# Optimization experiments

Hardware: AMD Instinct MI355X
Metric: run time of the kernel (lower is better)

## Reference

```python
import jax, jax.numpy as jnp
import numpy as np

N_TOKENS = 32768   # flattened batch*seq tokens
D = 1024           # expert_dim
E = 8              # num_experts
K = 2              # top_k


def setup_inputs() -> dict:
    key = jax.random.key(0)
    k0, k1, k2, k3, k4 = jax.random.split(key, 5)
    s = 1.0 / np.sqrt(D)  # torch Linear default init scale
    x = jax.random.normal(k0, (N_TOKENS, D), dtype=jnp.float32)
    gate_W = jax.random.normal(k1, (E, D), dtype=jnp.float32) * s
    gate_b = jax.random.uniform(k2, (E,), dtype=jnp.float32, minval=-s, maxval=s)
    expert_W = jax.random.normal(k3, (E, D, D), dtype=jnp.float32) * s
    expert_b = jax.random.uniform(k4, (E, D), dtype=jnp.float32, minval=-s, maxval=s)
    return {"x": x, "gate_W": gate_W, "gate_b": gate_b,
            "expert_W": expert_W, "expert_b": expert_b}


def reference(x, gate_W, gate_b, expert_W, expert_b):
    # Gating: logits [N, E] -> softmax -> top-k selection.
    logits = x @ gate_W.T + gate_b
    probs = jax.nn.softmax(logits, axis=-1)
    _, topk_idx = jax.lax.top_k(probs, K)                      # [N, K]
    # Combine weight = full softmax prob (NOT renormalized), zero if not in top-k.
    topk_mask = jax.nn.one_hot(topk_idx, E, dtype=probs.dtype).sum(axis=1)  # [N, E]
    w = probs * topk_mask                                       # [N, E]
    # Dense weighted dispatch/combine: mathematically identical to the
    # gather -> Linear -> scale -> scatter-add loop (w is 0 for unrouted experts).
    out = jnp.zeros_like(x)
    for e in range(E):  # fixed small structural loop over experts
        y_e = x @ expert_W[e].T + expert_b[e]                   # [N, D]
        out = out + w[:, e:e + 1] * y_e
    return out
```

## Files before the change

### kernel.cpp

```cpp
#include <hip/hip_runtime.h>
#include <hip/hip_bf16.h>
#include <cstdint>


#define N_TOK 32768
#define DIM   1024
#define NEXP  8
#define BM    128
#define BK    32
#define NTM   263

typedef __attribute__((ext_vector_type(8))) short short8;
typedef __attribute__((ext_vector_type(4))) float f32x4;
typedef unsigned short u16;

struct Ctrl {
  int counts[16];
  int cursors[16];
  int ntiles[2];
  int pad[30];
  int4 table[2 * NTM];
};

__device__ __forceinline__ void gload_lds16(void* lds, const void* g) {
  __builtin_amdgcn_global_load_lds(
      (const __attribute__((address_space(1))) void*)g,
      (__attribute__((address_space(3))) void*)lds, 16, 0, 0);
}

__device__ __forceinline__ void splitf(float f, u16& h, u16& l) {
  uint32_t u = __float_as_uint(f);
  h = (u16)(u >> 16);
  float r = f - __uint_as_float(u & 0xFFFF0000u);
  l = (u16)(__float_as_uint(r) >> 16);
}

extern "C" __global__ __launch_bounds__(256) void k_convert_w(
    const float4* __restrict__ W, ushort4* __restrict__ Wh, ushort4* __restrict__ Wl) {
  const int total = NEXP * DIM * DIM / 4;
  for (int i = blockIdx.x * 256 + threadIdx.x; i < total; i += gridDim.x * 256) {
    float4 v = W[i];
    u16 hx, lx, hy, ly, hz, lz, hw, lw;
    splitf(v.x, hx, lx); splitf(v.y, hy, ly);
    splitf(v.z, hz, lz); splitf(v.w, hw, lw);
    Wh[i] = make_ushort4(hx, hy, hz, hw);
    Wl[i] = make_ushort4(lx, ly, lz, lw);
  }
}

extern "C" __global__ __launch_bounds__(256) void k_gate(
    const float* __restrict__ x, const float* __restrict__ gW,
    const float* __restrict__ gb, u16* __restrict__ xh, u16* __restrict__ xl,
    float* __restrict__ wts, int* __restrict__ eids, int* __restrict__ counts) {
  __shared__ float4 gwl[NEXP * 256];
  __shared__ int cnt[16];
  int tid = threadIdx.x;
  for (int i = tid; i < NEXP * 256; i += 256) gwl[i] = ((const float4*)gW)[i];
  if (tid < 16) cnt[tid] = 0;
  __syncthreads();

  float gbr[NEXP];
#pragma unroll
  for (int e = 0; e < NEXP; ++e) gbr[e] = gb[e];

  int lane = tid & 63, wid = tid >> 6;
  int wave = blockIdx.x * 4 + wid;
  for (int t = wave; t < N_TOK; t += 2048) {
    const float4* xr = (const float4*)(x + (size_t)t * DIM);
    float acc[NEXP] = {0,0,0,0,0,0,0,0};
    float4 xv[4];
#pragma unroll
    for (int j = 0; j < 4; ++j) {
      float4 v = xr[j * 64 + lane];
      xv[j] = v;
#pragma unroll
      for (int e = 0; e < NEXP; ++e) {
        float4 g = gwl[e * 256 + j * 64 + lane];
        acc[e] += v.x * g.x + v.y * g.y + v.z * g.z + v.w * g.w;
      }
    }
#pragma unroll
    for (int off = 32; off > 0; off >>= 1)
#pragma unroll
      for (int e = 0; e < NEXP; ++e) acc[e] += __shfl_xor(acc[e], off, 64);

#pragma unroll
    for (int e = 0; e < NEXP; ++e) acc[e] += gbr[e];

    float m = acc[0];
#pragma unroll
    for (int e = 1; e < NEXP; ++e) m = fmaxf(m, acc[e]);
    float p[NEXP], s = 0.f;
#pragma unroll
    for (int e = 0; e < NEXP; ++e) { p[e] = expf(acc[e] - m); s += p[e]; }
    float inv = 1.f / s;

    int i0 = 0; float b0 = acc[0];
#pragma unroll
    for (int e = 1; e < NEXP; ++e) if (acc[e] > b0) { b0 = acc[e]; i0 = e; }
    int i1 = -1; float b1 = -3.4e38f;
#pragma unroll
    for (int e = 0; e < NEXP; ++e)
      if (e != i0 && acc[e] > b1) { b1 = acc[e]; i1 = e; }

    if (lane == 0) {
      wts[t * 2 + 0] = p[i0] * inv;
      wts[t * 2 + 1] = p[i1] * inv;
      eids[t * 2 + 0] = i0;
      eids[t * 2 + 1] = i1;
      atomicAdd(&cnt[i0], 1);
      atomicAdd(&cnt[8 + i1], 1);
    }
    ushort4* oh = (ushort4*)(xh + (size_t)t * DIM);
    ushort4* ol = (ushort4*)(xl + (size_t)t * DIM);
#pragma unroll
    for (int j = 0; j < 4; ++j) {
      u16 hx, lx, hy, ly, hz, lz, hw, lw;
      splitf(xv[j].x, hx, lx); splitf(xv[j].y, hy, ly);
      splitf(xv[j].z, hz, lz); splitf(xv[j].w, hw, lw);
      oh[j * 64 + lane] = make_ushort4(hx, hy, hz, hw);
      ol[j * 64 + lane] = make_ushort4(lx, ly, lz, lw);
    }
  }
  __syncthreads();
  if (tid < 16) atomicAdd(&counts[tid], cnt[tid]);
}

extern "C" __global__ void k_scan(Ctrl* ctrl) {
  if (threadIdx.x == 0) {
    for (int s = 0; s < 2; ++s) {
      int off = 0, nt = 0;
      for (int e = 0; e < NEXP; ++e) {
        int c = ctrl->counts[s * 8 + e];
        ctrl->cursors[s * 8 + e] = off;
        int tcnt = (c + BM - 1) >> 7;
        for (int i = 0; i < tcnt; ++i)
          ctrl->table[s * NTM + nt + i] =
              make_int4(e, off + i * BM, min(BM, c - i * BM), 0);
        nt += tcnt; off += c;
      }
      ctrl->ntiles[s] = nt;
    }
  }
}

extern "C" __global__ __launch_bounds__(256) void k_lists(
    const int* __restrict__ eids, int* __restrict__ cursors, int* __restrict__ lists) {
  int t = blockIdx.x * 256 + threadIdx.x;
  int lane = threadIdx.x & 63;
#pragma unroll
  for (int s = 0; s < 2; ++s) {
    int e = eids[t * 2 + s];
#pragma unroll
    for (int ex = 0; ex < NEXP; ++ex) {
      unsigned long long msk = __ballot(e == ex);
      if (msk) {
        int leader = __ffsll((unsigned long long)msk) - 1;
        int base = 0;
        if (lane == leader) base = atomicAdd(&cursors[s * 8 + ex], (int)__popcll(msk));
        base = __shfl(base, leader, 64);
        if (e == ex) {
          int pos = base + (int)__popcll(msk & ((1ull << lane) - 1ull));
          lists[s * N_TOK + pos] = t;
        }
      }
    }
  }
}

extern "C" __global__ __launch_bounds__(256) void k_gemm(
    int slot, const u16* __restrict__ xh, const u16* __restrict__ xl,
    const u16* __restrict__ Wh, const u16* __restrict__ Wl,
    const float* __restrict__ eb, const float* __restrict__ wts,
    const int* __restrict__ lists, const int* __restrict__ ntiles,
    const int4* __restrict__ table, float* __restrict__ out) {
  int tm = blockIdx.x >> 3, tn = blockIdx.x & 7;
  if (tm >= ntiles[slot]) return;
  int4 ent = table[slot * NTM + tm];
  int e = ent.x, start = ent.y, rows = ent.z;
  int n0 = tn * 128;

  __shared__ __align__(16) u16 Al[BM * BK];
  __shared__ __align__(16) u16 Bl[BM * BK];
  __shared__ int   tok[BM];
  __shared__ float wt[BM];

  int tid = threadIdx.x;
  if (tid < BM) {
    int t = 0; float w = 0.f;
    if (tid < rows) {
      t = lists[slot * N_TOK + start + tid];
      w = wts[t * 2 + slot];
    }
    tok[tid] = t; wt[tid] = w;
  }
  __syncthreads();

  int lane = tid & 63, wid = tid >> 6;
  int r0 = tid >> 2, seg = (tid & 3) * 8;
  int r1 = (tid + 256) >> 2;
  size_t aoff0 = (size_t)tok[r0] * DIM + seg;
  size_t aoff1 = (size_t)tok[r1] * DIM + seg;
  size_t boff0 = ((size_t)e * DIM + (n0 + r0)) * DIM + seg;
  size_t boff1 = ((size_t)e * DIM + (n0 + r1)) * DIM + seg;
  char* a_dst0 = (char*)Al + wid * 1024;
  char* a_dst1 = (char*)Al + 4096 + wid * 1024;
  char* b_dst0 = (char*)Bl + wid * 1024;
  char* b_dst1 = (char*)Bl + 4096 + wid * 1024;

  f32x4 acc[4][4] = {};
  int wm = wid >> 1, wn = wid & 1;
  int lrow = lane & 15, lk = (lane >> 4) * 8;

#pragma unroll 1
  for (int term = 0; term < 3; ++term) {
    const u16* asrc = (term == 2) ? xl : xh;
    const u16* bsrc = (term == 1) ? Wl : Wh;
    const u16* ap0 = asrc + aoff0;
    const u16* ap1 = asrc + aoff1;
    const u16* bp0 = bsrc + boff0;
    const u16* bp1 = bsrc + boff1;
#pragma unroll 1
    for (int col = 0; col < DIM; col += BK) {
      gload_lds16(a_dst0, ap0 + col);
      gload_lds16(a_dst1, ap1 + col);
      gload_lds16(b_dst0, bp0 + col);
      gload_lds16(b_dst1, bp1 + col);
      __syncthreads();

      short8 a[4], b[4];
#pragma unroll
      for (int mi = 0; mi < 4; ++mi)
        a[mi] = *(const short8*)&Al[(wm * 64 + mi * 16 + lrow) * BK + lk];
#pragma unroll
      for (int ni = 0; ni < 4; ++ni)
        b[ni] = *(const short8*)&Bl[(wn * 64 + ni * 16 + lrow) * BK + lk];
#pragma unroll
      for (int mi = 0; mi < 4; ++mi)
#pragma unroll
        for (int ni = 0; ni < 4; ++ni)
          acc[mi][ni] = __builtin_amdgcn_mfma_f32_16x16x32_bf16(
              a[mi], b[ni], acc[mi][ni], 0, 0, 0);
      __syncthreads();
    }
  }

#pragma unroll
  for (int mi = 0; mi < 4; ++mi) {
    int rbase = wm * 64 + mi * 16 + (lane >> 4) * 4;
#pragma unroll
    for (int ni = 0; ni < 4; ++ni) {
      int c = n0 + wn * 64 + ni * 16 + (lane & 15);
      float bv = eb[e * DIM + c];
#pragma unroll
      for (int j = 0; j < 4; ++j) {
        int r = rbase + j;
        if (r < rows) {
          float v = wt[r] * (acc[mi][ni][j] + bv);
          size_t oidx = (size_t)tok[r] * DIM + c;
          if (slot == 0) out[oidx] = v;
          else           out[oidx] += v;
        }
      }
    }
  }
}

extern "C" void kernel_launch(void* const* d_in, const int* in_sizes, int n_in,
                              void* d_out, int out_size, void* d_ws, size_t ws_size,
                              hipStream_t stream) {
  const float* x  = (const float*)d_in[0];
  const float* gW = (const float*)d_in[1];
  const float* gb = (const float*)d_in[2];
  const float* eW = (const float*)d_in[3];
  const float* eb = (const float*)d_in[4];
  float* out = (float*)d_out;

  char* ws = (char*)d_ws;
  size_t o = 0;
  u16* xh = (u16*)(ws + o); o += (size_t)N_TOK * DIM * 2;
  u16* xl = (u16*)(ws + o); o += (size_t)N_TOK * DIM * 2;
  u16* Wh = (u16*)(ws + o); o += (size_t)NEXP * DIM * DIM * 2;
  u16* Wl = (u16*)(ws + o); o += (size_t)NEXP * DIM * DIM * 2;
  float* wts = (float*)(ws + o); o += (size_t)N_TOK * 2 * 4;
  int* eids  = (int*)(ws + o);   o += (size_t)N_TOK * 2 * 4;
  int* lists = (int*)(ws + o);   o += (size_t)2 * N_TOK * 4;
  Ctrl* ctrl = (Ctrl*)(ws + o);  o += sizeof(Ctrl);

  hipMemsetAsync(ctrl->counts, 0, 16 * sizeof(int), stream);

  k_convert_w<<<2048, 256, 0, stream>>>((const float4*)eW, (ushort4*)Wh, (ushort4*)Wl);
  k_gate<<<512, 256, 0, stream>>>(x, gW, gb, xh, xl, wts, eids, ctrl->counts);
  k_scan<<<1, 64, 0, stream>>>(ctrl);
  k_lists<<<N_TOK / 256, 256, 0, stream>>>(eids, ctrl->cursors, lists);
  k_gemm<<<NTM * 8, 256, 0, stream>>>(0, xh, xl, Wh, Wl, eb, wts, lists,
                                      ctrl->ntiles, ctrl->table, out);
  k_gemm<<<NTM * 8, 256, 0, stream>>>(1, xh, xl, Wh, Wl, eb, wts, lists,
                                      ctrl->ntiles, ctrl->table, out);
}
```

Baseline: 1.102 ms.

## Rewrite grouped GEMM with 256x256 tiles, 4-stage LDS pipeline and swizzle

The grouped expert GEMM moves from 128x128 tiles with 256 threads and a synchronous single-buffer K loop to 256x256 tiles with 512 threads. It now runs a 4-deep global-to-LDS prefetch ring over a flattened 96-step K loop covering all three split-bf16 terms, uses an XOR swizzle on LDS offsets, and overlaps loads with MFMA half-steps using barriers, waitcnt and setprio. Blocks are remapped so neighbouring blocks share expert tiles, and the counts memset is folded into the weight-convert kernel. The aim is more data reuse per tile and hidden memory latency. The cost is 128KB of LDS per block, heavy register use, and more padding waste in expert tiles that are only partly filled.

```diff
diff --git a/kernel.cpp b/kernel.cpp
--- a/kernel.cpp
+++ b/kernel.cpp
@@ -6,9 +6,7 @@
 #define N_TOK 32768
 #define DIM   1024
 #define NEXP  8
-#define BM    128
-#define BK    32
-#define NTM   263
+#define NT2   136
 
 typedef __attribute__((ext_vector_type(8))) short short8;
 typedef __attribute__((ext_vector_type(4))) float f32x4;
@@ -19,7 +17,7 @@
   int cursors[16];
   int ntiles[2];
   int pad[30];
-  int4 table[2 * NTM];
+  int4 table[2 * NT2];
 };
 
 __device__ __forceinline__ void gload_lds16(void* lds, const void* g) {
@@ -36,7 +34,9 @@
 }
 
 extern "C" __global__ __launch_bounds__(256) void k_convert_w(
-    const float4* __restrict__ W, ushort4* __restrict__ Wh, ushort4* __restrict__ Wl) {
+    const float4* __restrict__ W, ushort4* __restrict__ Wh,
+    ushort4* __restrict__ Wl, int* __restrict__ counts) {
+  if (blockIdx.x == 0 && threadIdx.x < 16) counts[threadIdx.x] = 0;
   const int total = NEXP * DIM * DIM / 4;
   for (int i = blockIdx.x * 256 + threadIdx.x; i < total; i += gridDim.x * 256) {
     float4 v = W[i];
@@ -133,10 +133,10 @@
       for (int e = 0; e < NEXP; ++e) {
         int c = ctrl->counts[s * 8 + e];
         ctrl->cursors[s * 8 + e] = off;
-        int tcnt = (c + BM - 1) >> 7;
+        int tcnt = (c + 255) >> 8;
         for (int i = 0; i < tcnt; ++i)
-          ctrl->table[s * NTM + nt + i] =
-              make_int4(e, off + i * BM, min(BM, c - i * BM), 0);
+          ctrl->table[s * NT2 + nt + i] =
+              make_int4(e, off + i * 256, min(256, c - i * 256), 0);
         nt += tcnt; off += c;
       }
       ctrl->ntiles[s] = nt;
@@ -168,96 +168,132 @@
   }
 }
 
-extern "C" __global__ __launch_bounds__(256) void k_gemm(
+extern "C" __global__ __launch_bounds__(512, 2) void k_gemm(
     int slot, const u16* __restrict__ xh, const u16* __restrict__ xl,
     const u16* __restrict__ Wh, const u16* __restrict__ Wl,
     const float* __restrict__ eb, const float* __restrict__ wts,
     const int* __restrict__ lists, const int* __restrict__ ntiles,
     const int4* __restrict__ table, float* __restrict__ out) {
-  int tm = blockIdx.x >> 3, tn = blockIdx.x & 7;
+  int L = (blockIdx.x & 7) * (NT2 / 2) + (blockIdx.x >> 3);
+  int tm = L >> 2, tn = L & 3;
   if (tm >= ntiles[slot]) return;
-  int4 ent = table[slot * NTM + tm];
+  int4 ent = table[slot * NT2 + tm];
   int e = ent.x, start = ent.y, rows = ent.z;
-  int n0 = tn * 128;
-
-  __shared__ __align__(16) u16 Al[BM * BK];
-  __shared__ __align__(16) u16 Bl[BM * BK];
-  __shared__ int   tok[BM];
-  __shared__ float wt[BM];
-
-  int tid = threadIdx.x;
-  if (tid < BM) {
+  int n0 = tn * 256;
+
+  __shared__ __align__(16) char smemc[4 * 32768];
+  __shared__ int   tok_s[256];
+  __shared__ float wt_s[256];
+
+  int tid = threadIdx.x, lane = tid & 63, wid = tid >> 6;
+  if (tid < 256) {
     int t = 0; float w = 0.f;
-    if (tid < rows) {
-      t = lists[slot * N_TOK + start + tid];
-      w = wts[t * 2 + slot];
-    }
-    tok[tid] = t; wt[tid] = w;
+    if (tid < rows) { t = lists[slot * N_TOK + start + tid]; w = wts[t * 2 + slot]; }
+    tok_s[tid] = t; wt_s[tid] = w;
   }
   __syncthreads();
 
-  int lane = tid & 63, wid = tid >> 6;
-  int r0 = tid >> 2, seg = (tid & 3) * 8;
-  int r1 = (tid + 256) >> 2;
-  size_t aoff0 = (size_t)tok[r0] * DIM + seg;
-  size_t aoff1 = (size_t)tok[r1] * DIM + seg;
-  size_t boff0 = ((size_t)e * DIM + (n0 + r0)) * DIM + seg;
-  size_t boff1 = ((size_t)e * DIM + (n0 + r1)) * DIM + seg;
-  char* a_dst0 = (char*)Al + wid * 1024;
-  char* a_dst1 = (char*)Al + 4096 + wid * 1024;
-  char* b_dst0 = (char*)Bl + wid * 1024;
-  char* b_dst1 = (char*)Bl + 4096 + wid * 1024;
-
-  f32x4 acc[4][4] = {};
-  int wm = wid >> 1, wn = wid & 1;
-  int lrow = lane & 15, lk = (lane >> 4) * 8;
+  int fsw = ((lane & 3) ^ ((lane >> 2) & 3) ^ (lane >> 4)) << 4;
+
+  int rr = wid * 16 + (lane >> 2);
+  unsigned off_a0 = (unsigned)tok_s[rr] * 2048u + fsw;
+  unsigned off_a1 = (unsigned)tok_s[128 + rr] * 2048u + fsw;
+  unsigned off_b0 = (unsigned)((e << 10) + n0 + rr) * 2048u + fsw;
+  unsigned off_b1 = (unsigned)((e << 10) + n0 + 128 + rr) * 2048u + fsw;
+
+  int wm = wid >> 2, wn = wid & 3;
+  int aoff = wm * 8192 + (lane & 15) * 64 + fsw;
+  int boff = wn * 4096 + (lane & 15) * 64 + fsw;
+
+  f32x4 acc[8][4] = {};
+
+#pragma unroll
+  for (int t = 0; t < 3; ++t) {
+    const char* sA = (const char*)xh + t * 64;
+    const char* sB = (const char*)Wh + t * 64;
+    char* dst = smemc + t * 32768;
+    gload_lds16(dst +         wid * 1024, sA + off_a0);
+    gload_lds16(dst +  8192 + wid * 1024, sA + off_a1);
+    gload_lds16(dst + 16384 + wid * 1024, sB + off_b0);
+    gload_lds16(dst + 24576 + wid * 1024, sB + off_b1);
+  }
+  asm volatile("s_waitcnt vmcnt(8)" ::: "memory");
+  __builtin_amdgcn_s_barrier();
 
 #pragma unroll 1
-  for (int term = 0; term < 3; ++term) {
-    const u16* asrc = (term == 2) ? xl : xh;
-    const u16* bsrc = (term == 1) ? Wl : Wh;
-    const u16* ap0 = asrc + aoff0;
-    const u16* ap1 = asrc + aoff1;
-    const u16* bp0 = bsrc + boff0;
-    const u16* bp1 = bsrc + boff1;
-#pragma unroll 1
-    for (int col = 0; col < DIM; col += BK) {
-      gload_lds16(a_dst0, ap0 + col);
-      gload_lds16(a_dst1, ap1 + col);
-      gload_lds16(b_dst0, bp0 + col);
-      gload_lds16(b_dst1, bp1 + col);
-      __syncthreads();
-
-      short8 a[4], b[4];
-#pragma unroll
-      for (int mi = 0; mi < 4; ++mi)
-        a[mi] = *(const short8*)&Al[(wm * 64 + mi * 16 + lrow) * BK + lk];
+  for (int kt = 0; kt < 96; ++kt) {
+    int ks = kt + 3; if (ks > 95) ks = 95;
+    int termS = ks >> 5;
+    const char* sA = ((termS == 2) ? (const char*)xl : (const char*)xh) + ((ks & 31) << 6);
+    const char* sB = ((termS == 1) ? (const char*)Wl : (const char*)Wh) + ((ks & 31) << 6);
+    char* dst = smemc + ((kt + 3) & 3) * 32768;
+    const char* bufA = smemc + (kt & 3) * 32768;
+    const char* bufB = bufA + 16384;
+
+    short8 a[4], b[4];
+    gload_lds16(dst +         wid * 1024, sA + off_a0);
+    gload_lds16(dst + 16384 + wid * 1024, sB + off_b0);
+    {
+      const char* ap = bufA + aoff;
+      a[0] = *(const short8*)(ap);
+      a[1] = *(const short8*)(ap + 1024);
+      a[2] = *(const short8*)(ap + 2048);
+      a[3] = *(const short8*)(ap + 3072);
+      const char* bp = bufB + boff;
+      b[0] = *(const short8*)(bp);
+      b[1] = *(const short8*)(bp + 1024);
+      b[2] = *(const short8*)(bp + 2048);
+      b[3] = *(const short8*)(bp + 3072);
+    }
+    __builtin_amdgcn_s_barrier();
+    asm volatile("s_waitcnt lgkmcnt(0)" ::: "memory");
+    __builtin_amdgcn_sched_barrier(0);
+    __builtin_amdgcn_s_setprio(1);
+#pragma unroll
+    for (int mi = 0; mi < 4; ++mi)
 #pragma unroll
       for (int ni = 0; ni < 4; ++ni)
-        b[ni] = *(const short8*)&Bl[(wn * 64 + ni * 16 + lrow) * BK + lk];
-#pragma unroll
-      for (int mi = 0; mi < 4; ++mi)
-#pragma unroll
-        for (int ni = 0; ni < 4; ++ni)
-          acc[mi][ni] = __builtin_amdgcn_mfma_f32_16x16x32_bf16(
-              a[mi], b[ni], acc[mi][ni], 0, 0, 0);
-      __syncthreads();
-    }
-  }
-
-#pragma unroll
-  for (int mi = 0; mi < 4; ++mi) {
-    int rbase = wm * 64 + mi * 16 + (lane >> 4) * 4;
+        acc[mi][ni] = __builtin_amdgcn_mfma_f32_16x16x32_bf16(
+            a[mi], b[ni], acc[mi][ni], 0, 0, 0);
+    __builtin_amdgcn_s_setprio(0);
+    __builtin_amdgcn_s_barrier();
+    gload_lds16(dst +  8192 + wid * 1024, sA + off_a1);
+    gload_lds16(dst + 24576 + wid * 1024, sB + off_b1);
+    {
+      const char* ap = bufA + aoff + 4096;
+      a[0] = *(const short8*)(ap);
+      a[1] = *(const short8*)(ap + 1024);
+      a[2] = *(const short8*)(ap + 2048);
+      a[3] = *(const short8*)(ap + 3072);
+    }
+    __builtin_amdgcn_s_barrier();
+    asm volatile("s_waitcnt lgkmcnt(0)" ::: "memory");
+    __builtin_amdgcn_sched_barrier(0);
+    __builtin_amdgcn_s_setprio(1);
+#pragma unroll
+    for (int mi = 0; mi < 4; ++mi)
+#pragma unroll
+      for (int ni = 0; ni < 4; ++ni)
+        acc[4 + mi][ni] = __builtin_amdgcn_mfma_f32_16x16x32_bf16(
+            a[mi], b[ni], acc[4 + mi][ni], 0, 0, 0);
+    __builtin_amdgcn_s_setprio(0);
+    asm volatile("s_waitcnt vmcnt(8)" ::: "memory");
+    __builtin_amdgcn_s_barrier();
+  }
+
+#pragma unroll
+  for (int mi = 0; mi < 8; ++mi) {
+    int rb = wm * 128 + mi * 16 + (lane >> 4) * 4;
 #pragma unroll
     for (int ni = 0; ni < 4; ++ni) {
       int c = n0 + wn * 64 + ni * 16 + (lane & 15);
       float bv = eb[e * DIM + c];
 #pragma unroll
       for (int j = 0; j < 4; ++j) {
-        int r = rbase + j;
+        int r = rb + j;
         if (r < rows) {
-          float v = wt[r] * (acc[mi][ni][j] + bv);
-          size_t oidx = (size_t)tok[r] * DIM + c;
+          float v = wt_s[r] * (acc[mi][ni][j] + bv);
+          size_t oidx = (size_t)tok_s[r] * DIM + c;
           if (slot == 0) out[oidx] = v;
           else           out[oidx] += v;
         }
@@ -287,14 +323,13 @@
   int* lists = (int*)(ws + o);   o += (size_t)2 * N_TOK * 4;
   Ctrl* ctrl = (Ctrl*)(ws + o);  o += sizeof(Ctrl);
 
-  hipMemsetAsync(ctrl->counts, 0, 16 * sizeof(int), stream);
-
-  k_convert_w<<<2048, 256, 0, stream>>>((const float4*)eW, (ushort4*)Wh, (ushort4*)Wl);
+  k_convert_w<<<2048, 256, 0, stream>>>((const float4*)eW, (ushort4*)Wh,
+                                        (ushort4*)Wl, ctrl->counts);
   k_gate<<<512, 256, 0, stream>>>(x, gW, gb, xh, xl, wts, eids, ctrl->counts);
   k_scan<<<1, 64, 0, stream>>>(ctrl);
   k_lists<<<N_TOK / 256, 256, 0, stream>>>(eids, ctrl->cursors, lists);
-  k_gemm<<<NTM * 8, 256, 0, stream>>>(0, xh, xl, Wh, Wl, eb, wts, lists,
+  k_gemm<<<NT2 * 4, 512, 0, stream>>>(0, xh, xl, Wh, Wl, eb, wts, lists,
                                       ctrl->ntiles, ctrl->table, out);
-  k_gemm<<<NTM * 8, 256, 0, stream>>>(1, xh, xl, Wh, Wl, eb, wts, lists,
+  k_gemm<<<NT2 * 4, 512, 0, stream>>>(1, xh, xl, Wh, Wl, eb, wts, lists,
                                       ctrl->ntiles, ctrl->table, out);
 }
```

Result: slower. 1.470 ms (+33.4%).

## Double-buffer GEMM LDS tiles and fold counter memset into convert kernel

Applied to the files above, without the earlier changes.

Flattens the three split-bf16 term loops into one 96-step K loop with double-buffered LDS. The next tile is prefetched via global_load_lds while the current tile feeds the MFMAs, and one barrier per step is removed. The expert-count memset is also folded into the weight-conversion kernel to drop a separate API call. This doubles LDS usage per block, which may reduce occupancy, and the prefetch may still be forced to complete at the barrier.

```diff
diff --git a/kernel.cpp b/kernel.cpp
--- a/kernel.cpp
+++ b/kernel.cpp
@@ -36,7 +36,9 @@
 }
 
 extern "C" __global__ __launch_bounds__(256) void k_convert_w(
-    const float4* __restrict__ W, ushort4* __restrict__ Wh, ushort4* __restrict__ Wl) {
+    const float4* __restrict__ W, ushort4* __restrict__ Wh,
+    ushort4* __restrict__ Wl, int* __restrict__ counts) {
+  if (blockIdx.x == 0 && threadIdx.x < 16) counts[threadIdx.x] = 0;
   const int total = NEXP * DIM * DIM / 4;
   for (int i = blockIdx.x * 256 + threadIdx.x; i < total; i += gridDim.x * 256) {
     float4 v = W[i];
@@ -180,8 +182,8 @@
   int e = ent.x, start = ent.y, rows = ent.z;
   int n0 = tn * 128;
 
-  __shared__ __align__(16) u16 Al[BM * BK];
-  __shared__ __align__(16) u16 Bl[BM * BK];
+  __shared__ __align__(16) u16 Al[2][BM * BK];
+  __shared__ __align__(16) u16 Bl[2][BM * BK];
   __shared__ int   tok[BM];
   __shared__ float wt[BM];
 
@@ -203,46 +205,55 @@
   size_t aoff1 = (size_t)tok[r1] * DIM + seg;
   size_t boff0 = ((size_t)e * DIM + (n0 + r0)) * DIM + seg;
   size_t boff1 = ((size_t)e * DIM + (n0 + r1)) * DIM + seg;
-  char* a_dst0 = (char*)Al + wid * 1024;
-  char* a_dst1 = (char*)Al + 4096 + wid * 1024;
-  char* b_dst0 = (char*)Bl + wid * 1024;
-  char* b_dst1 = (char*)Bl + 4096 + wid * 1024;
+
+  char* A0 = (char*)&Al[0][0];
+  char* B0 = (char*)&Bl[0][0];
 
   f32x4 acc[4][4] = {};
   int wm = wid >> 1, wn = wid & 1;
   int lrow = lane & 15, lk = (lane >> 4) * 8;
 
+  {
+    gload_lds16(A0 +        wid * 1024, xh + aoff0);
+    gload_lds16(A0 + 4096 + wid * 1024, xh + aoff1);
+    gload_lds16(B0 +        wid * 1024, Wh + boff0);
+    gload_lds16(B0 + 4096 + wid * 1024, Wh + boff1);
+  }
+  __syncthreads();
+
+  int cur = 0;
 #pragma unroll 1
-  for (int term = 0; term < 3; ++term) {
-    const u16* asrc = (term == 2) ? xl : xh;
-    const u16* bsrc = (term == 1) ? Wl : Wh;
-    const u16* ap0 = asrc + aoff0;
-    const u16* ap1 = asrc + aoff1;
-    const u16* bp0 = bsrc + boff0;
-    const u16* bp1 = bsrc + boff1;
-#pragma unroll 1
-    for (int col = 0; col < DIM; col += BK) {
-      gload_lds16(a_dst0, ap0 + col);
-      gload_lds16(a_dst1, ap1 + col);
-      gload_lds16(b_dst0, bp0 + col);
-      gload_lds16(b_dst1, bp1 + col);
-      __syncthreads();
-
-      short8 a[4], b[4];
-#pragma unroll
-      for (int mi = 0; mi < 4; ++mi)
-        a[mi] = *(const short8*)&Al[(wm * 64 + mi * 16 + lrow) * BK + lk];
+  for (int kt = 0; kt < 96; ++kt) {
+    int ks = kt + 1; if (ks > 95) ks = 95;
+    {
+      int term = ks >> 5;
+      int colE = (ks & 31) * BK;
+      const u16* asrc = ((term == 2) ? xl : xh) + colE;
+      const u16* bsrc = ((term == 1) ? Wl : Wh) + colE;
+      char* dA = A0 + (cur ^ 1) * 8192;
+      char* dB = B0 + (cur ^ 1) * 8192;
+      gload_lds16(dA +        wid * 1024, asrc + aoff0);
+      gload_lds16(dA + 4096 + wid * 1024, asrc + aoff1);
+      gload_lds16(dB +        wid * 1024, bsrc + boff0);
+      gload_lds16(dB + 4096 + wid * 1024, bsrc + boff1);
+    }
+    const u16* As = &Al[cur][0];
+    const u16* Bs = &Bl[cur][0];
+    short8 a[4], b[4];
+#pragma unroll
+    for (int mi = 0; mi < 4; ++mi)
+      a[mi] = *(const short8*)&As[(wm * 64 + mi * 16 + lrow) * BK + lk];
+#pragma unroll
+    for (int ni = 0; ni < 4; ++ni)
+      b[ni] = *(const short8*)&Bs[(wn * 64 + ni * 16 + lrow) * BK + lk];
+#pragma unroll
+    for (int mi = 0; mi < 4; ++mi)
 #pragma unroll
       for (int ni = 0; ni < 4; ++ni)
-        b[ni] = *(const short8*)&Bl[(wn * 64 + ni * 16 + lrow) * BK + lk];
-#pragma unroll
-      for (int mi = 0; mi < 4; ++mi)
-#pragma unroll
-        for (int ni = 0; ni < 4; ++ni)
-          acc[mi][ni] = __builtin_amdgcn_mfma_f32_16x16x32_bf16(
-              a[mi], b[ni], acc[mi][ni], 0, 0, 0);
-      __syncthreads();
-    }
+        acc[mi][ni] = __builtin_amdgcn_mfma_f32_16x16x32_bf16(
+            a[mi], b[ni], acc[mi][ni], 0, 0, 0);
+    __syncthreads();
+    cur ^= 1;
   }
 
 #pragma unroll
@@ -287,9 +298,8 @@
   int* lists = (int*)(ws + o);   o += (size_t)2 * N_TOK * 4;
   Ctrl* ctrl = (Ctrl*)(ws + o);  o += sizeof(Ctrl);
 
-  hipMemsetAsync(ctrl->counts, 0, 16 * sizeof(int), stream);
-
-  k_convert_w<<<2048, 256, 0, stream>>>((const float4*)eW, (ushort4*)Wh, (ushort4*)Wl);
+  k_convert_w<<<2048, 256, 0, stream>>>((const float4*)eW, (ushort4*)Wh,
+                                        (ushort4*)Wl, ctrl->counts);
   k_gate<<<512, 256, 0, stream>>>(x, gW, gb, xh, xl, wts, eids, ctrl->counts);
   k_scan<<<1, 64, 0, stream>>>(ctrl);
   k_lists<<<N_TOK / 256, 256, 0, stream>>>(eids, ctrl->cursors, lists);
```

After: 1.229 ms. +11.6%, slower.
